# Kernel tuning notes

Measured on AMD Instinct MI355X. Metric: run time of the kernel, lower is better.

The kernel has to match this reference:

```python
import jax, jax.numpy as jnp
import numpy as np

B, S, D, H = 4, 2048, 512, 8
HD = D // H  # head_dim = 64


def setup_inputs() -> dict:
    key = jax.random.key(0)
    ks = jax.random.split(key, 10)
    scale = 1.0 / np.sqrt(D)  # keep activations O(1)
    x = jax.random.normal(ks[0], (B, S, D), dtype=jnp.float32)
    # causal mask, broadcast over batch and heads
    causal = jnp.tril(jnp.ones((S, S), dtype=bool))
    mask = jnp.broadcast_to(causal, (B, H, S, S))
    def lin(k):
        return jax.random.normal(k, (D, D), dtype=jnp.float32) * scale
    return {
        "x": x,
        "mask": mask,
        "Wq": lin(ks[1]), "bq": jax.random.normal(ks[2], (D,), dtype=jnp.float32) * 0.01,
        "Wk": lin(ks[3]), "bk": jax.random.normal(ks[4], (D,), dtype=jnp.float32) * 0.01,
        "Wv": lin(ks[5]), "bv": jax.random.normal(ks[6], (D,), dtype=jnp.float32) * 0.01,
        "Wo": lin(ks[7]), "bo": jax.random.normal(ks[8], (D,), dtype=jnp.float32) * 0.01,
    }


def reference(x, mask, Wq, bq, Wk, bk, Wv, bv, Wo, bo):
    # eqx.nn.Linear computes W @ x + b per row; batched form is x @ W.T + b.
    b, s, d = x.shape
    q = jnp.einsum("bsd,ed->bse", x, Wq) + bq
    k = jnp.einsum("bsd,ed->bse", x, Wk) + bk
    v = jnp.einsum("bsd,ed->bse", x, Wv) + bv
    # [B, H, S, HD]
    q = q.reshape(b, s, H, HD).transpose(0, 2, 1, 3)
    k = k.reshape(b, s, H, HD).transpose(0, 2, 1, 3)
    v = v.reshape(b, s, H, HD).transpose(0, 2, 1, 3)
    scores = jnp.einsum("bhqd,bhkd->bhqk", q, k) / jnp.sqrt(jnp.asarray(HD, x.dtype))
    scores = jnp.where(mask, scores, jnp.asarray(-1e9, x.dtype))
    attn = jax.nn.softmax(scores, axis=-1)
    attended = jnp.einsum("bhqk,bhkd->bhqd", attn, v)
    attended = attended.transpose(0, 2, 1, 3).reshape(b, s, d)
    out = jnp.einsum("bsd,ed->bse", attended, Wo) + bo
    return out
```

## Files before the change

### kernel.cpp

```cpp
#include <hip/hip_runtime.h>

#define S_LEN 2048
#define DM    512
#define NH    8
#define HD    64

typedef unsigned short u16;
typedef unsigned int   u32;
typedef __bf16 bf16_t;
typedef bf16_t bf16x8 __attribute__((ext_vector_type(8)));
typedef float  f32x4  __attribute__((ext_vector_type(4)));

__device__ __forceinline__ u16 f2bf(float f) {
    u32 u = __float_as_uint(f);
    u += 0x7FFFu + ((u >> 16) & 1u);
    return (u16)(u >> 16);
}

__device__ __forceinline__ float qmax16(float v) {
    v = fmaxf(v, __shfl_xor(v, 1));
    v = fmaxf(v, __shfl_xor(v, 2));
    v = fmaxf(v, __shfl_xor(v, 4));
    v = fmaxf(v, __shfl_xor(v, 8));
    return v;
}
__device__ __forceinline__ float qsum16(float v) {
    v += __shfl_xor(v, 1);
    v += __shfl_xor(v, 2);
    v += __shfl_xor(v, 4);
    v += __shfl_xor(v, 8);
    return v;
}

__global__ __launch_bounds__(256) void cvt_bf16(
    const float* __restrict__ x,
    const float* __restrict__ wq, const float* __restrict__ wk,
    const float* __restrict__ wv, const float* __restrict__ wo,
    u16* __restrict__ xb, u16* __restrict__ wqb, u16* __restrict__ wkb,
    u16* __restrict__ wvb, u16* __restrict__ wob)
{
    const int y = blockIdx.y;
    const float* src; u16* dst; int n;
    if (y == 0)      { src = x;  dst = xb;  n = 4 * S_LEN * DM; }
    else if (y == 1) { src = wq; dst = wqb; n = DM * DM; }
    else if (y == 2) { src = wk; dst = wkb; n = DM * DM; }
    else if (y == 3) { src = wv; dst = wvb; n = DM * DM; }
    else             { src = wo; dst = wob; n = DM * DM; }
    int idx = (blockIdx.x * 256 + threadIdx.x) * 8;
    if (idx >= n) return;
    float4 f0 = *(const float4*)(src + idx);
    float4 f1 = *(const float4*)(src + idx + 4);
    u32 p0 = (u32)f2bf(f0.x) | ((u32)f2bf(f0.y) << 16);
    u32 p1 = (u32)f2bf(f0.z) | ((u32)f2bf(f0.w) << 16);
    u32 p2 = (u32)f2bf(f1.x) | ((u32)f2bf(f1.y) << 16);
    u32 p3 = (u32)f2bf(f1.z) | ((u32)f2bf(f1.w) << 16);
    *(uint4*)(dst + idx) = make_uint4(p0, p1, p2, p3);
}

__global__ __launch_bounds__(256) void qkv_gemm(
    const u16* __restrict__ xb,
    const u16* __restrict__ Wqb, const u16* __restrict__ Wkb, const u16* __restrict__ Wvb,
    const float* __restrict__ bq, const float* __restrict__ bk, const float* __restrict__ bv,
    u16* __restrict__ Qb, u16* __restrict__ Kb, u16* __restrict__ Vb)
{
    __shared__ u16 Als[4096];
    __shared__ u16 Bls[4096];

    const int t = threadIdx.x;
    const int lane = t & 63, w = t >> 6;
    const int ln = lane & 15, quad = lane >> 4;
    const int wm = w >> 1, wn = w & 1;
    const int m0 = blockIdx.x * 128;
    const int mat = blockIdx.y >> 2;
    const int n0 = (blockIdx.y & 3) * 128;

    const u16* __restrict__ Wb    = (mat == 0) ? Wqb : (mat == 1) ? Wkb : Wvb;
    const float* __restrict__ bias = (mat == 0) ? bq : (mat == 1) ? bk : bv;
    u16* __restrict__ outp         = (mat == 0) ? Qb : (mat == 1) ? Kb : Vb;

    const int c0 = t, c1 = t + 256;
    const int r0 = c0 >> 2, kq0 = c0 & 3, ch0 = r0 * 4 + (kq0 ^ ((r0 >> 1) & 3));
    const int r1 = c1 >> 2, kq1 = c1 & 3, ch1 = r1 * 4 + (kq1 ^ ((r1 >> 1) & 3));

    f32x4 acc[4][4] = {};
    for (int k0 = 0; k0 < DM; k0 += 32) {
        uint4 a0 = *(const uint4*)(xb + (size_t)(m0 + r0) * DM + k0 + kq0 * 8);
        uint4 a1 = *(const uint4*)(xb + (size_t)(m0 + r1) * DM + k0 + kq1 * 8);
        uint4 b0 = *(const uint4*)(Wb + (size_t)(n0 + r0) * DM + k0 + kq0 * 8);
        uint4 b1 = *(const uint4*)(Wb + (size_t)(n0 + r1) * DM + k0 + kq1 * 8);
        __syncthreads();
        *(uint4*)(Als + ch0 * 8) = a0;
        *(uint4*)(Als + ch1 * 8) = a1;
        *(uint4*)(Bls + ch0 * 8) = b0;
        *(uint4*)(Bls + ch1 * 8) = b1;
        __syncthreads();
        bf16x8 af[4], bf8[4];
        #pragma unroll
        for (int i = 0; i < 4; ++i) {
            int row = wm * 64 + i * 16 + ln;
            af[i] = *(const bf16x8*)(Als + (row * 4 + (quad ^ ((row >> 1) & 3))) * 8);
        }
        #pragma unroll
        for (int j = 0; j < 4; ++j) {
            int row = wn * 64 + j * 16 + ln;
            bf8[j] = *(const bf16x8*)(Bls + (row * 4 + (quad ^ ((row >> 1) & 3))) * 8);
        }
        #pragma unroll
        for (int i = 0; i < 4; ++i)
            #pragma unroll
            for (int j = 0; j < 4; ++j)
                acc[i][j] = __builtin_amdgcn_mfma_f32_16x16x32_bf16(af[i], bf8[j], acc[i][j], 0, 0, 0);
    }

    #pragma unroll
    for (int j = 0; j < 4; ++j) {
        int colg = n0 + wn * 64 + j * 16 + ln;
        float bj = bias[colg];
        int h = colg >> 6, d = colg & 63;
        #pragma unroll
        for (int i = 0; i < 4; ++i) {
            int mbase = m0 + wm * 64 + i * 16 + quad * 4;
            #pragma unroll
            for (int r = 0; r < 4; ++r) {
                int m = mbase + r;
                int bb = m >> 11, s = m & 2047;
                outp[(((size_t)bb * NH + h) * S_LEN + s) * HD + d] = f2bf(acc[i][j][r] + bj);
            }
        }
    }
}

__global__ __launch_bounds__(256) void attn_mfma(
    const u16* __restrict__ Qb, const u16* __restrict__ Kb, const u16* __restrict__ Vb,
    u16* __restrict__ Attb)
{
    __shared__ u16 Qls[8192];
    __shared__ u16 Kls[4096];
    __shared__ u16 Vt[4096];
    __shared__ u16 Ps[8192];

    const int t = threadIdx.x;
    const int lane = t & 63, w = t >> 6;
    const int ln = lane & 15, quad = lane >> 4;
    const int qt = blockIdx.x, bh = blockIdx.y;
    const int q_base = qt * 128;
    const size_t base = (size_t)bh * S_LEN * HD;

    #pragma unroll
    for (int cc = 0; cc < 4; ++cc) {
        int c = t + cc * 256;
        int row = c >> 3, kq = c & 7;
        uint4 v = *(const uint4*)(Qb + base + (size_t)(q_base + row) * HD + kq * 8);
        *(uint4*)(Qls + (row * 8 + (kq ^ (row & 7))) * 8) = v;
    }
    __syncthreads();

    bf16x8 aq[2][2];
    #pragma unroll
    for (int i = 0; i < 2; ++i)
        #pragma unroll
        for (int ks = 0; ks < 2; ++ks) {
            int row = w * 32 + i * 16 + ln;
            int kqg = ks * 4 + quad;
            aq[i][ks] = *(const bf16x8*)(Qls + (row * 8 + (kqg ^ (row & 7))) * 8);
        }

    float m_st[2][4], l_st[2][4];
    f32x4 o[2][4] = {};
    #pragma unroll
    for (int i = 0; i < 2; ++i)
        #pragma unroll
        for (int r = 0; r < 4; ++r) { m_st[i][r] = -1e30f; l_st[i][r] = 0.f; }

    const int ktmax = (q_base + 127) >> 6;
    const int qrow0 = q_base + w * 32;

    for (int kt = 0; kt <= ktmax; ++kt) {
        #pragma unroll
        for (int cc = 0; cc < 2; ++cc) {
            int c = t + cc * 256;
            int row = c >> 3, kq = c & 7;
            uint4 v = *(const uint4*)(Kb + base + (size_t)(kt * 64 + row) * HD + kq * 8);
            *(uint4*)(Kls + (row * 8 + (kq ^ (row & 7))) * 8) = v;
        }
        #pragma unroll
        for (int cc = 0; cc < 2; ++cc) {
            int c = t + cc * 256;
            int kv = c >> 3, d0 = (c & 7) * 8;
            uint4 vv = *(const uint4*)(Vb + base + (size_t)(kt * 64 + kv) * HD + d0);
            u16 ve[8];
            *(uint4*)ve = vv;
            int kvq = kv >> 3, kvl = kv & 7;
            #pragma unroll
            for (int ii = 0; ii < 8; ++ii) {
                int i = (ii + (t & 7)) & 7;
                int d = d0 + i;
                Vt[(d * 8 + (kvq ^ (d & 7))) * 8 + kvl] = ve[i];
            }
        }
        __syncthreads();

        f32x4 s[2][4] = {};
        #pragma unroll
        for (int ks = 0; ks < 2; ++ks)
            #pragma unroll
            for (int j = 0; j < 4; ++j) {
                int row = j * 16 + ln;
                int kqg = ks * 4 + quad;
                bf16x8 bk8 = *(const bf16x8*)(Kls + (row * 8 + (kqg ^ (row & 7))) * 8);
                #pragma unroll
                for (int i = 0; i < 2; ++i)
                    s[i][j] = __builtin_amdgcn_mfma_f32_16x16x32_bf16(aq[i][ks], bk8, s[i][j], 0, 0, 0);
            }

        bool need_mask = (kt * 64 + 63) > qrow0;
        #pragma unroll
        for (int i = 0; i < 2; ++i)
            #pragma unroll
            for (int j = 0; j < 4; ++j)
                #pragma unroll
                for (int r = 0; r < 4; ++r) {
                    float sv = s[i][j][r] * 0.125f;
                    if (need_mask) {
                        int qg = qrow0 + i * 16 + quad * 4 + r;
                        int kg = kt * 64 + j * 16 + ln;
                        if (kg > qg) sv = -1e30f;
                    }
                    s[i][j][r] = sv;
                }

        float alpha[2][4];
        #pragma unroll
        for (int i = 0; i < 2; ++i)
            #pragma unroll
            for (int r = 0; r < 4; ++r) {
                float mx = fmaxf(fmaxf(s[i][0][r], s[i][1][r]), fmaxf(s[i][2][r], s[i][3][r]));
                mx = qmax16(mx);
                float mnew = fmaxf(m_st[i][r], mx);
                float al = __expf(m_st[i][r] - mnew);
                m_st[i][r] = mnew;
                float rs = 0.f;
                #pragma unroll
                for (int j = 0; j < 4; ++j) {
                    float p = __expf(s[i][j][r] - mnew);
                    s[i][j][r] = p;
                    rs += p;
                }
                rs = qsum16(rs);
                l_st[i][r] = l_st[i][r] * al + rs;
                alpha[i][r] = al;
            }
        #pragma unroll
        for (int i = 0; i < 2; ++i)
            #pragma unroll
            for (int j = 0; j < 4; ++j)
                #pragma unroll
                for (int r = 0; r < 4; ++r)
                    o[i][j][r] *= alpha[i][r];

        #pragma unroll
        for (int i = 0; i < 2; ++i)
            #pragma unroll
            for (int j = 0; j < 4; ++j) {
                int key = j * 16 + ln;
                int kq = key >> 3, kl = key & 7;
                #pragma unroll
                for (int r = 0; r < 4; ++r) {
                    int qloc = w * 32 + i * 16 + quad * 4 + r;
                    Ps[(qloc * 8 + (kq ^ (qloc & 7))) * 8 + kl] = f2bf(s[i][j][r]);
                }
            }

        #pragma unroll
        for (int ks = 0; ks < 2; ++ks) {
            int kqg = ks * 4 + quad;
            bf16x8 pa[2];
            #pragma unroll
            for (int i = 0; i < 2; ++i) {
                int row = w * 32 + i * 16 + ln;
                pa[i] = *(const bf16x8*)(Ps + (row * 8 + (kqg ^ (row & 7))) * 8);
            }
            #pragma unroll
            for (int j = 0; j < 4; ++j) {
                int rowd = j * 16 + ln;
                bf16x8 vb8 = *(const bf16x8*)(Vt + (rowd * 8 + (kqg ^ (rowd & 7))) * 8);
                #pragma unroll
                for (int i = 0; i < 2; ++i)
                    o[i][j] = __builtin_amdgcn_mfma_f32_16x16x32_bf16(pa[i], vb8, o[i][j], 0, 0, 0);
            }
        }
        __syncthreads();
    }

    const int bb = bh >> 3, h = bh & 7;
    #pragma unroll
    for (int i = 0; i < 2; ++i)
        #pragma unroll
        for (int r = 0; r < 4; ++r) {
            int qg = qrow0 + i * 16 + quad * 4 + r;
            float inv = 1.f / l_st[i][r];
            #pragma unroll
            for (int j = 0; j < 4; ++j) {
                int d = j * 16 + ln;
                Attb[((size_t)(bb * S_LEN + qg)) * DM + h * HD + d] = f2bf(o[i][j][r] * inv);
            }
        }
}

__global__ __launch_bounds__(256) void out_gemm(
    const u16* __restrict__ Ab, const u16* __restrict__ Wob,
    const float* __restrict__ bo, float* __restrict__ out)
{
    __shared__ u16 Als[4096];
    __shared__ u16 Bls[4096];

    const int t = threadIdx.x;
    const int lane = t & 63, w = t >> 6;
    const int ln = lane & 15, quad = lane >> 4;
    const int wm = w >> 1, wn = w & 1;
    const int m0 = blockIdx.x * 128;
    const int n0 = blockIdx.y * 128;

    const int c0 = t, c1 = t + 256;
    const int r0 = c0 >> 2, kq0 = c0 & 3, ch0 = r0 * 4 + (kq0 ^ ((r0 >> 1) & 3));
    const int r1 = c1 >> 2, kq1 = c1 & 3, ch1 = r1 * 4 + (kq1 ^ ((r1 >> 1) & 3));

    f32x4 acc[4][4] = {};
    for (int k0 = 0; k0 < DM; k0 += 32) {
        uint4 a0 = *(const uint4*)(Ab + (size_t)(m0 + r0) * DM + k0 + kq0 * 8);
        uint4 a1 = *(const uint4*)(Ab + (size_t)(m0 + r1) * DM + k0 + kq1 * 8);
        uint4 b0 = *(const uint4*)(Wob + (size_t)(n0 + r0) * DM + k0 + kq0 * 8);
        uint4 b1 = *(const uint4*)(Wob + (size_t)(n0 + r1) * DM + k0 + kq1 * 8);
        __syncthreads();
        *(uint4*)(Als + ch0 * 8) = a0;
        *(uint4*)(Als + ch1 * 8) = a1;
        *(uint4*)(Bls + ch0 * 8) = b0;
        *(uint4*)(Bls + ch1 * 8) = b1;
        __syncthreads();
        bf16x8 af[4], bf8[4];
        #pragma unroll
        for (int i = 0; i < 4; ++i) {
            int row = wm * 64 + i * 16 + ln;
            af[i] = *(const bf16x8*)(Als + (row * 4 + (quad ^ ((row >> 1) & 3))) * 8);
        }
        #pragma unroll
        for (int j = 0; j < 4; ++j) {
            int row = wn * 64 + j * 16 + ln;
            bf8[j] = *(const bf16x8*)(Bls + (row * 4 + (quad ^ ((row >> 1) & 3))) * 8);
        }
        #pragma unroll
        for (int i = 0; i < 4; ++i)
            #pragma unroll
            for (int j = 0; j < 4; ++j)
                acc[i][j] = __builtin_amdgcn_mfma_f32_16x16x32_bf16(af[i], bf8[j], acc[i][j], 0, 0, 0);
    }

    #pragma unroll
    for (int j = 0; j < 4; ++j) {
        int colg = n0 + wn * 64 + j * 16 + ln;
        float bj = bo[colg];
        #pragma unroll
        for (int i = 0; i < 4; ++i) {
            int mbase = m0 + wm * 64 + i * 16 + quad * 4;
            #pragma unroll
            for (int r = 0; r < 4; ++r) {
                int m = mbase + r;
                out[(size_t)m * DM + colg] = acc[i][j][r] + bj;
            }
        }
    }
}

extern "C" void kernel_launch(void* const* d_in, const int* in_sizes, int n_in,
                              void* d_out, int out_size, void* d_ws, size_t ws_size,
                              hipStream_t stream) {
    const float* x  = (const float*)d_in[0];
    const float* Wq = (const float*)d_in[2];
    const float* bq = (const float*)d_in[3];
    const float* Wk = (const float*)d_in[4];
    const float* bk = (const float*)d_in[5];
    const float* Wv = (const float*)d_in[6];
    const float* bv = (const float*)d_in[7];
    const float* Wo = (const float*)d_in[8];
    const float* bo = (const float*)d_in[9];
    float* out = (float*)d_out;

    u16* ws = (u16*)d_ws;
    const size_t NX = (size_t)4 * S_LEN * DM;
    const size_t NW = (size_t)DM * DM;
    u16* xb   = ws;
    u16* wqb  = xb + NX;
    u16* wkb  = wqb + NW;
    u16* wvb  = wkb + NW;
    u16* wob  = wvb + NW;
    u16* Qb   = wob + NW;
    u16* Kb   = Qb + NX;
    u16* Vb   = Kb + NX;
    u16* Attb = Vb + NX;

    cvt_bf16<<<dim3(2048, 5), 256, 0, stream>>>(x, Wq, Wk, Wv, Wo, xb, wqb, wkb, wvb, wob);
    qkv_gemm<<<dim3(64, 12), 256, 0, stream>>>(xb, wqb, wkb, wvb, bq, bk, bv, Qb, Kb, Vb);
    attn_mfma<<<dim3(16, 32), 256, 0, stream>>>(Qb, Kb, Vb, Attb);
    out_gemm<<<dim3(64, 4), 256, 0, stream>>>(Attb, wob, bo, out);
}
```

Measured before the change: 765.8 us.

## Use direct global-to-LDS loads and halve attention query tile to 64

Replaces register-staged global loads with global_load_lds (16-byte) in both GEMMs and the attention kernel, so tiles land straight in LDS with a pre-swizzled source address. The attention kernel moves from 128-row to 64-row query tiles, doubling the grid to 1024 blocks with rotated tile order for load balance, and now masks only the diagonal tile. It also switches to exp2 with the log2e factor folded into the scale. The intent is to cut VGPR pressure and load latency and to raise occupancy. In exchange there is less K/V reuse per block, and correctness depends on the direct-to-LDS lane layout and on the trailing barrier moving to the top of the loop.

```diff
diff --git a/kernel.cpp b/kernel.cpp
--- a/kernel.cpp
+++ b/kernel.cpp
@@ -15,6 +15,13 @@
     u32 u = __float_as_uint(f);
     u += 0x7FFFu + ((u >> 16) & 1u);
     return (u16)(u >> 16);
+}
+
+__device__ __forceinline__ void g2l16(const u16* g, u16* l) {
+    __builtin_amdgcn_global_load_lds(
+        (const __attribute__((address_space(1))) u32*)g,
+        (__attribute__((address_space(3))) u32*)l,
+        16, 0, 0);
 }
 
 __device__ __forceinline__ float qmax16(float v) {
@@ -74,25 +81,33 @@
     const int mat = blockIdx.y >> 2;
     const int n0 = (blockIdx.y & 3) * 128;
 
-    const u16* __restrict__ Wb    = (mat == 0) ? Wqb : (mat == 1) ? Wkb : Wvb;
+    const u16* __restrict__ Wb     = (mat == 0) ? Wqb : (mat == 1) ? Wkb : Wvb;
     const float* __restrict__ bias = (mat == 0) ? bq : (mat == 1) ? bk : bv;
     u16* __restrict__ outp         = (mat == 0) ? Qb : (mat == 1) ? Kb : Vb;
 
-    const int c0 = t, c1 = t + 256;
-    const int r0 = c0 >> 2, kq0 = c0 & 3, ch0 = r0 * 4 + (kq0 ^ ((r0 >> 1) & 3));
-    const int r1 = c1 >> 2, kq1 = c1 & 3, ch1 = r1 * 4 + (kq1 ^ ((r1 >> 1) & 3));
+    const int ch0 = (w * 2 + 0) * 64 + lane;
+    const int ch1 = (w * 2 + 1) * 64 + lane;
+    const int sr0 = ch0 >> 2, sk0 = (ch0 & 3) ^ ((sr0 >> 1) & 3);
+    const int sr1 = ch1 >> 2, sk1 = (ch1 & 3) ^ ((sr1 >> 1) & 3);
+    const u16* pA0 = xb + (size_t)(m0 + sr0) * DM + sk0 * 8;
+    const u16* pA1 = xb + (size_t)(m0 + sr1) * DM + sk1 * 8;
+    const u16* pB0 = Wb + (size_t)(n0 + sr0) * DM + sk0 * 8;
+    const u16* pB1 = Wb + (size_t)(n0 + sr1) * DM + sk1 * 8;
+    u16* lds0 = (u16*)((w * 2 + 0) * 512);
+    u16* lds1 = (u16*)((w * 2 + 1) * 512);
+    u16* lA0 = Als + (w * 2 + 0) * 512;
+    u16* lA1 = Als + (w * 2 + 1) * 512;
+    u16* lB0 = Bls + (w * 2 + 0) * 512;
+    u16* lB1 = Bls + (w * 2 + 1) * 512;
+    (void)lds0; (void)lds1;
 
     f32x4 acc[4][4] = {};
     for (int k0 = 0; k0 < DM; k0 += 32) {
-        uint4 a0 = *(const uint4*)(xb + (size_t)(m0 + r0) * DM + k0 + kq0 * 8);
-        uint4 a1 = *(const uint4*)(xb + (size_t)(m0 + r1) * DM + k0 + kq1 * 8);
-        uint4 b0 = *(const uint4*)(Wb + (size_t)(n0 + r0) * DM + k0 + kq0 * 8);
-        uint4 b1 = *(const uint4*)(Wb + (size_t)(n0 + r1) * DM + k0 + kq1 * 8);
-        __syncthreads();
-        *(uint4*)(Als + ch0 * 8) = a0;
-        *(uint4*)(Als + ch1 * 8) = a1;
-        *(uint4*)(Bls + ch0 * 8) = b0;
-        *(uint4*)(Bls + ch1 * 8) = b1;
+        __syncthreads();
+        g2l16(pA0 + k0, lA0);
+        g2l16(pA1 + k0, lA1);
+        g2l16(pB0 + k0, lB0);
+        g2l16(pB1 + k0, lB1);
         __syncthreads();
         bf16x8 af[4], bf8[4];
         #pragma unroll
@@ -134,177 +149,172 @@
     const u16* __restrict__ Qb, const u16* __restrict__ Kb, const u16* __restrict__ Vb,
     u16* __restrict__ Attb)
 {
-    __shared__ u16 Qls[8192];
+    __shared__ u16 Qls[4096];
     __shared__ u16 Kls[4096];
     __shared__ u16 Vt[4096];
-    __shared__ u16 Ps[8192];
+    __shared__ u16 Ps[4096];
 
     const int t = threadIdx.x;
     const int lane = t & 63, w = t >> 6;
     const int ln = lane & 15, quad = lane >> 4;
-    const int qt = blockIdx.x, bh = blockIdx.y;
-    const int q_base = qt * 128;
+    const int bh = blockIdx.y;
+    const int qt = (blockIdx.x + bh) & 31;
+    const int q_base = qt * 64;
     const size_t base = (size_t)bh * S_LEN * HD;
 
+    {
+        const int c0 = (w * 2 + 0) * 64 + lane;
+        const int c1 = (w * 2 + 1) * 64 + lane;
+        const int r0 = c0 >> 3, k0 = (c0 & 7) ^ (r0 & 7);
+        const int r1 = c1 >> 3, k1 = (c1 & 7) ^ (r1 & 7);
+        g2l16(Qb + base + (size_t)(q_base + r0) * HD + k0 * 8, Qls + (w * 2 + 0) * 512);
+        g2l16(Qb + base + (size_t)(q_base + r1) * HD + k1 * 8, Qls + (w * 2 + 1) * 512);
+    }
+    __syncthreads();
+
+    bf16x8 aq[2];
     #pragma unroll
-    for (int cc = 0; cc < 4; ++cc) {
-        int c = t + cc * 256;
-        int row = c >> 3, kq = c & 7;
-        uint4 v = *(const uint4*)(Qb + base + (size_t)(q_base + row) * HD + kq * 8);
-        *(uint4*)(Qls + (row * 8 + (kq ^ (row & 7))) * 8) = v;
-    }
-    __syncthreads();
-
-    bf16x8 aq[2][2];
+    for (int ks = 0; ks < 2; ++ks) {
+        int row = w * 16 + ln;
+        aq[ks] = *(const bf16x8*)(Qls + (row * 8 + ((ks * 4 + quad) ^ (row & 7))) * 8);
+    }
+
+    const int ck0 = (w * 2 + 0) * 64 + lane;
+    const int ck1 = (w * 2 + 1) * 64 + lane;
+    const int kr0 = ck0 >> 3, kk0 = (ck0 & 7) ^ (kr0 & 7);
+    const int kr1 = ck1 >> 3, kk1 = (ck1 & 7) ^ (kr1 & 7);
+    const u16* pK0 = Kb + base + (size_t)kr0 * HD + kk0 * 8;
+    const u16* pK1 = Kb + base + (size_t)kr1 * HD + kk1 * 8;
+    u16* lK0 = Kls + (w * 2 + 0) * 512;
+    u16* lK1 = Kls + (w * 2 + 1) * 512;
+
+    const int vkey0 = t >> 3,        vd0 = (t & 7) * 8;
+    const int vkey1 = (t + 256) >> 3;
+    const u16* pV0 = Vb + base + (size_t)vkey0 * HD + vd0;
+    const u16* pV1 = Vb + base + (size_t)vkey1 * HD + vd0;
+
+    float m_st[4], l_st[4], alpha[4];
+    f32x4 o[4] = {};
     #pragma unroll
-    for (int i = 0; i < 2; ++i)
-        #pragma unroll
-        for (int ks = 0; ks < 2; ++ks) {
-            int row = w * 32 + i * 16 + ln;
-            int kqg = ks * 4 + quad;
-            aq[i][ks] = *(const bf16x8*)(Qls + (row * 8 + (kqg ^ (row & 7))) * 8);
-        }
-
-    float m_st[2][4], l_st[2][4];
-    f32x4 o[2][4] = {};
-    #pragma unroll
-    for (int i = 0; i < 2; ++i)
-        #pragma unroll
-        for (int r = 0; r < 4; ++r) { m_st[i][r] = -1e30f; l_st[i][r] = 0.f; }
-
-    const int ktmax = (q_base + 127) >> 6;
-    const int qrow0 = q_base + w * 32;
-
-    for (int kt = 0; kt <= ktmax; ++kt) {
-        #pragma unroll
-        for (int cc = 0; cc < 2; ++cc) {
-            int c = t + cc * 256;
-            int row = c >> 3, kq = c & 7;
-            uint4 v = *(const uint4*)(Kb + base + (size_t)(kt * 64 + row) * HD + kq * 8);
-            *(uint4*)(Kls + (row * 8 + (kq ^ (row & 7))) * 8) = v;
-        }
-        #pragma unroll
-        for (int cc = 0; cc < 2; ++cc) {
-            int c = t + cc * 256;
-            int kv = c >> 3, d0 = (c & 7) * 8;
-            uint4 vv = *(const uint4*)(Vb + base + (size_t)(kt * 64 + kv) * HD + d0);
+    for (int r = 0; r < 4; ++r) { m_st[r] = -1e30f; l_st[r] = 0.f; }
+
+    const float sc = 0.125f * 1.44269504f;
+    const int qrow_base = q_base + w * 16;
+
+    for (int kt = 0; kt <= qt; ++kt) {
+        __syncthreads();
+        g2l16(pK0 + (size_t)kt * 64 * HD, lK0);
+        g2l16(pK1 + (size_t)kt * 64 * HD, lK1);
+        {
+            uint4 vv0 = *(const uint4*)(pV0 + (size_t)kt * 64 * HD);
+            uint4 vv1 = *(const uint4*)(pV1 + (size_t)kt * 64 * HD);
             u16 ve[8];
-            *(uint4*)ve = vv;
-            int kvq = kv >> 3, kvl = kv & 7;
+            *(uint4*)ve = vv0;
+            int kvq = vkey0 >> 3, kvl = vkey0 & 7;
             #pragma unroll
             for (int ii = 0; ii < 8; ++ii) {
                 int i = (ii + (t & 7)) & 7;
-                int d = d0 + i;
+                int d = vd0 + i;
                 Vt[(d * 8 + (kvq ^ (d & 7))) * 8 + kvl] = ve[i];
             }
-        }
-        __syncthreads();
-
-        f32x4 s[2][4] = {};
+            *(uint4*)ve = vv1;
+            kvq = vkey1 >> 3; kvl = vkey1 & 7;
+            #pragma unroll
+            for (int ii = 0; ii < 8; ++ii) {
+                int i = (ii + (t & 7)) & 7;
+                int d = vd0 + i;
+                Vt[(d * 8 + (kvq ^ (d & 7))) * 8 + kvl] = ve[i];
+            }
+        }
+        __syncthreads();
+
+        f32x4 s[4] = {};
         #pragma unroll
         for (int ks = 0; ks < 2; ++ks)
             #pragma unroll
             for (int j = 0; j < 4; ++j) {
-                int row = j * 16 + ln;
-                int kqg = ks * 4 + quad;
-                bf16x8 bk8 = *(const bf16x8*)(Kls + (row * 8 + (kqg ^ (row & 7))) * 8);
-                #pragma unroll
-                for (int i = 0; i < 2; ++i)
-                    s[i][j] = __builtin_amdgcn_mfma_f32_16x16x32_bf16(aq[i][ks], bk8, s[i][j], 0, 0, 0);
-            }
-
-        bool need_mask = (kt * 64 + 63) > qrow0;
-        #pragma unroll
-        for (int i = 0; i < 2; ++i)
+                int krow = j * 16 + ln;
+                bf16x8 bk8 = *(const bf16x8*)(Kls + (krow * 8 + ((ks * 4 + quad) ^ (krow & 7))) * 8);
+                s[j] = __builtin_amdgcn_mfma_f32_16x16x32_bf16(aq[ks], bk8, s[j], 0, 0, 0);
+            }
+
+        if (kt == qt) {
             #pragma unroll
             for (int j = 0; j < 4; ++j)
                 #pragma unroll
                 for (int r = 0; r < 4; ++r) {
-                    float sv = s[i][j][r] * 0.125f;
-                    if (need_mask) {
-                        int qg = qrow0 + i * 16 + quad * 4 + r;
-                        int kg = kt * 64 + j * 16 + ln;
-                        if (kg > qg) sv = -1e30f;
-                    }
-                    s[i][j][r] = sv;
+                    int qg = qrow_base + quad * 4 + r;
+                    int kg = kt * 64 + j * 16 + ln;
+                    s[j][r] = (kg > qg) ? -1e30f : s[j][r] * sc;
                 }
-
-        float alpha[2][4];
-        #pragma unroll
-        for (int i = 0; i < 2; ++i)
-            #pragma unroll
-            for (int r = 0; r < 4; ++r) {
-                float mx = fmaxf(fmaxf(s[i][0][r], s[i][1][r]), fmaxf(s[i][2][r], s[i][3][r]));
-                mx = qmax16(mx);
-                float mnew = fmaxf(m_st[i][r], mx);
-                float al = __expf(m_st[i][r] - mnew);
-                m_st[i][r] = mnew;
-                float rs = 0.f;
-                #pragma unroll
-                for (int j = 0; j < 4; ++j) {
-                    float p = __expf(s[i][j][r] - mnew);
-                    s[i][j][r] = p;
-                    rs += p;
-                }
-                rs = qsum16(rs);
-                l_st[i][r] = l_st[i][r] * al + rs;
-                alpha[i][r] = al;
-            }
-        #pragma unroll
-        for (int i = 0; i < 2; ++i)
+        } else {
             #pragma unroll
             for (int j = 0; j < 4; ++j)
                 #pragma unroll
                 for (int r = 0; r < 4; ++r)
-                    o[i][j][r] *= alpha[i][r];
-
-        #pragma unroll
-        for (int i = 0; i < 2; ++i)
+                    s[j][r] *= sc;
+        }
+
+        #pragma unroll
+        for (int r = 0; r < 4; ++r) {
+            float mx = fmaxf(fmaxf(s[0][r], s[1][r]), fmaxf(s[2][r], s[3][r]));
+            mx = qmax16(mx);
+            float mnew = fmaxf(m_st[r], mx);
+            float al = __builtin_amdgcn_exp2f(m_st[r] - mnew);
+            m_st[r] = mnew;
+            float rs = 0.f;
             #pragma unroll
             for (int j = 0; j < 4; ++j) {
-                int key = j * 16 + ln;
-                int kq = key >> 3, kl = key & 7;
-                #pragma unroll
-                for (int r = 0; r < 4; ++r) {
-                    int qloc = w * 32 + i * 16 + quad * 4 + r;
-                    Ps[(qloc * 8 + (kq ^ (qloc & 7))) * 8 + kl] = f2bf(s[i][j][r]);
-                }
-            }
+                float p = __builtin_amdgcn_exp2f(s[j][r] - mnew);
+                s[j][r] = p;
+                rs += p;
+            }
+            rs = qsum16(rs);
+            l_st[r] = l_st[r] * al + rs;
+            alpha[r] = al;
+        }
+        #pragma unroll
+        for (int j = 0; j < 4; ++j)
+            #pragma unroll
+            for (int r = 0; r < 4; ++r)
+                o[j][r] *= alpha[r];
+
+        #pragma unroll
+        for (int j = 0; j < 4; ++j) {
+            int key = j * 16 + ln;
+            int kq = key >> 3, kl = key & 7;
+            #pragma unroll
+            for (int r = 0; r < 4; ++r) {
+                int qrow = w * 16 + quad * 4 + r;
+                Ps[(qrow * 8 + (kq ^ (qrow & 7))) * 8 + kl] = f2bf(s[j][r]);
+            }
+        }
 
         #pragma unroll
         for (int ks = 0; ks < 2; ++ks) {
             int kqg = ks * 4 + quad;
-            bf16x8 pa[2];
-            #pragma unroll
-            for (int i = 0; i < 2; ++i) {
-                int row = w * 32 + i * 16 + ln;
-                pa[i] = *(const bf16x8*)(Ps + (row * 8 + (kqg ^ (row & 7))) * 8);
-            }
+            int prow = w * 16 + ln;
+            bf16x8 pa = *(const bf16x8*)(Ps + (prow * 8 + (kqg ^ (prow & 7))) * 8);
             #pragma unroll
             for (int j = 0; j < 4; ++j) {
                 int rowd = j * 16 + ln;
                 bf16x8 vb8 = *(const bf16x8*)(Vt + (rowd * 8 + (kqg ^ (rowd & 7))) * 8);
-                #pragma unroll
-                for (int i = 0; i < 2; ++i)
-                    o[i][j] = __builtin_amdgcn_mfma_f32_16x16x32_bf16(pa[i], vb8, o[i][j], 0, 0, 0);
-            }
-        }
-        __syncthreads();
+                o[j] = __builtin_amdgcn_mfma_f32_16x16x32_bf16(pa, vb8, o[j], 0, 0, 0);
+            }
+        }
     }
 
     const int bb = bh >> 3, h = bh & 7;
     #pragma unroll
-    for (int i = 0; i < 2; ++i)
-        #pragma unroll
-        for (int r = 0; r < 4; ++r) {
-            int qg = qrow0 + i * 16 + quad * 4 + r;
-            float inv = 1.f / l_st[i][r];
-            #pragma unroll
-            for (int j = 0; j < 4; ++j) {
-                int d = j * 16 + ln;
-                Attb[((size_t)(bb * S_LEN + qg)) * DM + h * HD + d] = f2bf(o[i][j][r] * inv);
-            }
-        }
+    for (int r = 0; r < 4; ++r) {
+        int qg = q_base + w * 16 + quad * 4 + r;
+        float inv = 1.f / l_st[r];
+        #pragma unroll
+        for (int j = 0; j < 4; ++j) {
+            int d = j * 16 + ln;
+            Attb[((size_t)(bb * S_LEN + qg)) * DM + h * HD + d] = f2bf(o[j][r] * inv);
+        }
+    }
 }
 
 __global__ __launch_bounds__(256) void out_gemm(
@@ -321,21 +331,26 @@
     const int m0 = blockIdx.x * 128;
     const int n0 = blockIdx.y * 128;
 
-    const int c0 = t, c1 = t + 256;
-    const int r0 = c0 >> 2, kq0 = c0 & 3, ch0 = r0 * 4 + (kq0 ^ ((r0 >> 1) & 3));
-    const int r1 = c1 >> 2, kq1 = c1 & 3, ch1 = r1 * 4 + (kq1 ^ ((r1 >> 1) & 3));
+    const int ch0 = (w * 2 + 0) * 64 + lane;
+    const int ch1 = (w * 2 + 1) * 64 + lane;
+    const int sr0 = ch0 >> 2, sk0 = (ch0 & 3) ^ ((sr0 >> 1) & 3);
+    const int sr1 = ch1 >> 2, sk1 = (ch1 & 3) ^ ((sr1 >> 1) & 3);
+    const u16* pA0 = Ab  + (size_t)(m0 + sr0) * DM + sk0 * 8;
+    const u16* pA1 = Ab  + (size_t)(m0 + sr1) * DM + sk1 * 8;
+    const u16* pB0 = Wob + (size_t)(n0 + sr0) * DM + sk0 * 8;
+    const u16* pB1 = Wob + (size_t)(n0 + sr1) * DM + sk1 * 8;
+    u16* lA0 = Als + (w * 2 + 0) * 512;
+    u16* lA1 = Als + (w * 2 + 1) * 512;
+    u16* lB0 = Bls + (w * 2 + 0) * 512;
+    u16* lB1 = Bls + (w * 2 + 1) * 512;
 
     f32x4 acc[4][4] = {};
     for (int k0 = 0; k0 < DM; k0 += 32) {
-        uint4 a0 = *(const uint4*)(Ab + (size_t)(m0 + r0) * DM + k0 + kq0 * 8);
-        uint4 a1 = *(const uint4*)(Ab + (size_t)(m0 + r1) * DM + k0 + kq1 * 8);
-        uint4 b0 = *(const uint4*)(Wob + (size_t)(n0 + r0) * DM + k0 + kq0 * 8);
-        uint4 b1 = *(const uint4*)(Wob + (size_t)(n0 + r1) * DM + k0 + kq1 * 8);
-        __syncthreads();
-        *(uint4*)(Als + ch0 * 8) = a0;
-        *(uint4*)(Als + ch1 * 8) = a1;
-        *(uint4*)(Bls + ch0 * 8) = b0;
-        *(uint4*)(Bls + ch1 * 8) = b1;
+        __syncthreads();
+        g2l16(pA0 + k0, lA0);
+        g2l16(pA1 + k0, lA1);
+        g2l16(pB0 + k0, lB0);
+        g2l16(pB1 + k0, lB1);
         __syncthreads();
         bf16x8 af[4], bf8[4];
         #pragma unroll
@@ -400,6 +415,6 @@
 
     cvt_bf16<<<dim3(2048, 5), 256, 0, stream>>>(x, Wq, Wk, Wv, Wo, xb, wqb, wkb, wvb, wob);
     qkv_gemm<<<dim3(64, 12), 256, 0, stream>>>(xb, wqb, wkb, wvb, bq, bk, bv, Qb, Kb, Vb);
-    attn_mfma<<<dim3(16, 32), 256, 0, stream>>>(Qb, Kb, Vb, Attb);
+    attn_mfma<<<dim3(32, 32), 256, 0, stream>>>(Qb, Kb, Vb, Attb);
     out_gemm<<<dim3(64, 4), 256, 0, stream>>>(Attb, wob, bo, out);
 }
```

After: 776.4 us. Within noise of the previous version (+1.4%).
